# Kernel optimization log

Hardware: AMD Instinct MI355X
Metric: run time of the kernel (lower is better)

## Reference

```python
import jax, jax.numpy as jnp
import numpy as np

NUM_HEADS = 16
ROPE_THETA = 10000.0


def _rotate_half(x):
    d = x.shape[-1] // 2
    return jnp.concatenate((-x[..., d:], x[..., :d]), axis=-1)


def setup_inputs() -> dict:
    key = jax.random.key(0)
    k1, k2, k3, k4 = jax.random.split(key, 4)
    T, HID = 3072, 1024
    hidden_states = jax.random.normal(k1, (T, HID), dtype=jnp.float32)
    w_qkv = jax.random.normal(k2, (HID, 3 * HID), dtype=jnp.float32) * (1.0 / np.sqrt(HID))
    w_o = jax.random.normal(k3, (HID, HID), dtype=jnp.float32) * (1.0 / np.sqrt(HID))
    attention_mask = jnp.zeros((T, T), dtype=jnp.float32)  # additive bias over token pairs
    position_ids = jax.random.randint(k4, (T,), 0, T, dtype=jnp.int32)
    return {
        "hidden_states": hidden_states,
        "w_qkv": w_qkv,
        "w_o": w_o,
        "attention_mask": attention_mask,
        "position_ids": position_ids,
    }


def reference(hidden_states, w_qkv, w_o, attention_mask, position_ids):
    T, hid = hidden_states.shape
    H = NUM_HEADS
    D = hid // H

    # fused QKV projection (bias=False)
    qkv = hidden_states @ w_qkv  # [T, 3*hid]
    q, k, v = jnp.split(qkv, 3, axis=-1)
    q = q.reshape(T, H, D)
    k = k.reshape(T, H, D)
    v = v.reshape(T, H, D)

    # RoPE per packed-token position_ids
    inv_freq = 1.0 / (ROPE_THETA ** (jnp.arange(0, D, 2, dtype=jnp.float32) / D))  # [D/2]
    freqs = position_ids.astype(jnp.float32)[:, None] * inv_freq[None, :]  # [T, D/2]
    emb = jnp.concatenate((freqs, freqs), axis=-1)  # [T, D]
    cos = jnp.cos(emb)[:, None, :]  # [T, 1, D]
    sin = jnp.sin(emb)[:, None, :]
    q = q * cos + _rotate_half(q) * sin
    k = k * cos + _rotate_half(k) * sin

    # dense token-token attention over packed tokens
    scale = 1.0 / np.sqrt(D).astype(np.float32)
    scores = jnp.einsum("thd,shd->hts", q, k) * scale  # [H, T, T]
    scores = scores + attention_mask[None, :, :]
    probs = jax.nn.softmax(scores, axis=-1)
    out = jnp.einsum("hts,shd->thd", probs, v).reshape(T, hid)
    return out @ w_o
```

## Files before the change

kernel.cpp:

```cpp
#include <hip/hip_runtime.h>
#include <hip/hip_bf16.h>
#include <hip/hip_fp16.h>
#include <math.h>

#define T_TOK 3072
#define HID   1024
#define NH    16
#define HD    64
#define KVSPLIT 4
#define KVCHUNK (T_TOK / KVSPLIT)
#define NQB (T_TOK / 128)
#define LOG2E 1.4426950408889634f

typedef __attribute__((ext_vector_type(8))) short bf16x8;
typedef __attribute__((ext_vector_type(8))) unsigned short u16x8;
typedef __attribute__((ext_vector_type(4))) float f32x4;
typedef __attribute__((ext_vector_type(16))) float f32x16;
typedef __attribute__((ext_vector_type(4))) unsigned int u32x4;

#define VMCNT(n) asm volatile("s_waitcnt vmcnt(" #n ")" ::: "memory")
#define SB() __builtin_amdgcn_sched_barrier(0)

static __device__ __forceinline__ unsigned short f2bf(float x) {
  __hip_bfloat16 h = __float2bfloat16(x);
  return __builtin_bit_cast(unsigned short, h);
}
static __device__ __forceinline__ float bf2f(unsigned short u) {
  unsigned int v = (unsigned int)u << 16;
  return __builtin_bit_cast(float, v);
}
static __device__ __forceinline__ unsigned short f2h(float x) {
  __half h = __float2half(x);
  return __builtin_bit_cast(unsigned short, h);
}
static __device__ __forceinline__ float h2f(unsigned short u) {
  __half h = __builtin_bit_cast(__half, u);
  return __half2float(h);
}

static __device__ __forceinline__ int swz(int row, int cb) {
  return row * 64 + ((cb ^ ((row & 7) << 4)) >> 1);
}

__global__ __launch_bounds__(256) void prep(const float* __restrict__ X,
                                            const float* __restrict__ Wqkv,
                                            const float* __restrict__ Wo,
                                            const int* __restrict__ pos,
                                            const float* __restrict__ mask,
                                            unsigned short* __restrict__ Xb,
                                            unsigned short* __restrict__ WqkvT,
                                            unsigned short* __restrict__ WoT,
                                            float* __restrict__ ctab,
                                            float* __restrict__ stab,
                                            int* __restrict__ flags) {
  __shared__ float tile[32][33];
  __shared__ int sflag;
  const int b = blockIdx.x;
  const int tid = threadIdx.x;
  if (b < 3072) {
    int i = (b * 256 + tid) * 4;
    float4 v = *(const float4*)(X + i);
    ushort4 o;
    o.x = f2bf(v.x); o.y = f2bf(v.y); o.z = f2bf(v.z); o.w = f2bf(v.w);
    *(ushort4*)(Xb + i) = o;
  } else if (b < 6144) {
    int b2 = b - 3072;
    int c0 = (b2 % 96) * 32, r0 = (b2 / 96) * 32;
    int tx = tid & 31, ty = tid >> 5;
    #pragma unroll
    for (int i2 = 0; i2 < 32; i2 += 8)
      tile[ty + i2][tx] = Wqkv[(size_t)(r0 + ty + i2) * 3072 + c0 + tx];
    __syncthreads();
    #pragma unroll
    for (int i2 = 0; i2 < 32; i2 += 8)
      WqkvT[(size_t)(c0 + ty + i2) * 1024 + r0 + tx] = f2bf(tile[tx][ty + i2]);
  } else if (b < 7168) {
    int b2 = b - 6144;
    int c0 = (b2 % 32) * 32, r0 = (b2 / 32) * 32;
    int tx = tid & 31, ty = tid >> 5;
    #pragma unroll
    for (int i2 = 0; i2 < 32; i2 += 8)
      tile[ty + i2][tx] = Wo[(size_t)(r0 + ty + i2) * 1024 + c0 + tx];
    __syncthreads();
    #pragma unroll
    for (int i2 = 0; i2 < 32; i2 += 8)
      WoT[(size_t)(c0 + ty + i2) * 1024 + r0 + tx] = f2bf(tile[tx][ty + i2]);
  } else if (b < 7552) {
    int i = (b - 7168) * 256 + tid;
    int t = i >> 5, j = i & 31;
    float inv = expf(-(float)j * 0.28782313662425572f);
    float f = (float)pos[t] * inv;
    ctab[i] = cosf(f);
    stab[i] = sinf(f);
  } else {
    int c = b - 7552;
    int qx = c % NQB, z = c / NQB;
    const float* base = mask + (size_t)(qx * 128) * T_TOK + z * KVCHUNK;
    int any = 0;
    const int NC4 = KVCHUNK / 4;
    for (int i = tid; i < 128 * NC4; i += 256) {
      int row = i / NC4, cc = i - row * NC4;
      float4 v = *(const float4*)(base + (size_t)row * T_TOK + cc * 4);
      any |= (v.x != 0.f) | (v.y != 0.f) | (v.z != 0.f) | (v.w != 0.f);
    }
    if (tid == 0) sflag = 0;
    __syncthreads();
    if (__any(any) && (tid & 63) == 0) sflag = 1;
    __syncthreads();
    if (tid == 0) flags[z * NQB + qx] = sflag;
  }
}

__global__ __launch_bounds__(256) void rope_v(const unsigned short* __restrict__ QKVb,
                                              const float* __restrict__ ctab,
                                              const float* __restrict__ stab,
                                              unsigned short* __restrict__ Qh,
                                              unsigned short* __restrict__ Kh,
                                              unsigned short* __restrict__ Vt) {
  const float QSCL = 0.18033688011112042f;
  const int h = blockIdx.y;
  const int t0 = blockIdx.x * 64;
  const int g = threadIdx.x & 3, tl = threadIdx.x >> 2;
  const int t = t0 + tl;
  __shared__ unsigned short vlds[64][72];

  const size_t rowb = (size_t)t * (3 * HID) + h * HD + g * 8;
  u16x8 qa = *(const u16x8*)(QKVb + rowb);
  u16x8 qb = *(const u16x8*)(QKVb + rowb + 32);
  u16x8 ka = *(const u16x8*)(QKVb + rowb + HID);
  u16x8 kb = *(const u16x8*)(QKVb + rowb + HID + 32);
  u16x8 va = *(const u16x8*)(QKVb + rowb + 2 * HID);
  u16x8 vb = *(const u16x8*)(QKVb + rowb + 2 * HID + 32);

  u16x8 qo0, qo1, ko0, ko1;
  #pragma unroll
  for (int e = 0; e < 8; ++e) {
    int j = g * 8 + e;
    float c = ctab[t * 32 + j], s = stab[t * 32 + j];
    float q1 = bf2f(qa[e]), q2 = bf2f(qb[e]);
    float k1 = bf2f(ka[e]), k2 = bf2f(kb[e]);
    qo0[e] = f2bf((q1 * c - q2 * s) * QSCL);
    qo1[e] = f2bf((q2 * c + q1 * s) * QSCL);
    ko0[e] = f2bf(k1 * c - k2 * s);
    ko1[e] = f2bf(k2 * c + k1 * s);
    vlds[tl][j] = va[e];
    vlds[tl][32 + j] = vb[e];
  }
  size_t ob = ((size_t)h * T_TOK + t) * HD + g * 8;
  *(u16x8*)(Qh + ob) = qo0;
  *(u16x8*)(Qh + ob + 32) = qo1;
  *(u16x8*)(Kh + ob) = ko0;
  *(u16x8*)(Kh + ob + 32) = ko1;

  __syncthreads();
  u16x8 o0, o1;
  #pragma unroll
  for (int e = 0; e < 8; ++e) {
    o0[e] = vlds[g * 16 + e][tl];
    o1[e] = vlds[g * 16 + 8 + e][tl];
  }
  u16x8 w0, w1;
  #pragma unroll
  for (int e = 0; e < 4; ++e) {
    w0[e] = o0[e];     w0[4 + e] = o1[e];
    w1[e] = o0[4 + e]; w1[4 + e] = o1[4 + e];
  }
  size_t vb2 = ((size_t)h * HD + tl) * T_TOK + t0 + g * 16;
  *(u16x8*)(Vt + vb2) = w0;
  *(u16x8*)(Vt + vb2 + 8) = w1;
}

template <int OBF16>
__device__ __forceinline__ void gemm_body(const unsigned short* __restrict__ A,
                                          const unsigned short* __restrict__ Bt,
                                          float* __restrict__ C,
                                          unsigned short* __restrict__ Cb,
                                          int M, int N, int K) {
  __shared__ unsigned short As[2][128 * 32];
  __shared__ unsigned short Bs[2][128 * 32];
  const int lane = threadIdx.x & 63;
  const int wv = threadIdx.x >> 6;
  const int wm = wv >> 1, wn = wv & 1;
  const int r = lane & 15, hi = lane >> 4;
  const int nwg = gridDim.x;
  const int flat = blockIdx.x;
  const int sid = (flat & 7) * (nwg >> 3) + (flat >> 3);
  const int mblocks = M >> 7;
  const int m0 = (sid % mblocks) * 128, n0 = (sid / mblocks) * 128;

  const int srow = lane >> 2;
  const int scb  = ((lane & 3) * 16) ^ ((srow & 3) << 4);
  const unsigned short* ga = A  + (size_t)(m0 + wv * 16 + srow) * K + (scb >> 1);
  const unsigned short* gb = Bt + (size_t)(n0 + wv * 16 + srow) * K + (scb >> 1);
  char* asd = (char*)&As[0][0] + wv * 1024;
  char* bsd = (char*)&Bs[0][0] + wv * 1024;

  auto stage = [&](int buf, int kt) {
    __builtin_amdgcn_global_load_lds(
        (const __attribute__((address_space(1))) unsigned int*)(ga + kt),
        (__attribute__((address_space(3))) unsigned int*)(asd + buf * 8192), 16, 0, 0);
    __builtin_amdgcn_global_load_lds(
        (const __attribute__((address_space(1))) unsigned int*)(ga + (size_t)64 * K + kt),
        (__attribute__((address_space(3))) unsigned int*)(asd + buf * 8192 + 4096), 16, 0, 0);
    __builtin_amdgcn_global_load_lds(
        (const __attribute__((address_space(1))) unsigned int*)(gb + kt),
        (__attribute__((address_space(3))) unsigned int*)(bsd + buf * 8192), 16, 0, 0);
    __builtin_amdgcn_global_load_lds(
        (const __attribute__((address_space(1))) unsigned int*)(gb + (size_t)64 * K + kt),
        (__attribute__((address_space(3))) unsigned int*)(bsd + buf * 8192 + 4096), 16, 0, 0);
  };

  f32x4 acc[4][4] = {};
  const int NT = K >> 5;
  stage(0, 0);
  #pragma unroll 2
  for (int it = 0; it < NT; ++it) {
    const int buf = it & 1;
    if (it + 1 < NT) {
      stage(buf ^ 1, (it + 1) * 32);
      VMCNT(4);
    } else {
      VMCNT(0);
    }
    SB();
    __builtin_amdgcn_s_barrier();
    SB();
    bf16x8 a[4], b[4];
    const int cbs = (hi * 16) ^ ((r & 3) << 4);
    #pragma unroll
    for (int tm = 0; tm < 4; ++tm)
      a[tm] = *(const bf16x8*)&As[buf][(wm * 64 + tm * 16 + r) * 32 + (cbs >> 1)];
    #pragma unroll
    for (int tn = 0; tn < 4; ++tn)
      b[tn] = *(const bf16x8*)&Bs[buf][(wn * 64 + tn * 16 + r) * 32 + (cbs >> 1)];
    #pragma unroll
    for (int tm = 0; tm < 4; ++tm)
      #pragma unroll
      for (int tn = 0; tn < 4; ++tn)
        acc[tm][tn] = __builtin_amdgcn_mfma_f32_16x16x32_bf16(a[tm], b[tn], acc[tm][tn], 0, 0, 0);
    __builtin_amdgcn_s_barrier();
  }
  #pragma unroll
  for (int tm = 0; tm < 4; ++tm)
    #pragma unroll
    for (int tn = 0; tn < 4; ++tn) {
      int colg = n0 + wn * 64 + tn * 16 + r;
      int rowg = m0 + wm * 64 + tm * 16 + hi * 4;
      if (OBF16) {
        unsigned short* cp = Cb + (size_t)rowg * N + colg;
        #pragma unroll
        for (int j = 0; j < 4; ++j) cp[(size_t)j * N] = f2bf(acc[tm][tn][j]);
      } else {
        float* cp = C + (size_t)rowg * N + colg;
        #pragma unroll
        for (int j = 0; j < 4; ++j) cp[(size_t)j * N] = acc[tm][tn][j];
      }
    }
}

__global__ __launch_bounds__(256) void gemm_bt(const unsigned short* __restrict__ A,
                                               const unsigned short* __restrict__ Bt,
                                               float* __restrict__ C, int M, int N, int K) {
  gemm_body<0>(A, Bt, C, nullptr, M, N, K);
}
__global__ __launch_bounds__(256) void gemm_bt_bf16(const unsigned short* __restrict__ A,
                                                    const unsigned short* __restrict__ Bt,
                                                    unsigned short* __restrict__ Cb,
                                                    int M, int N, int K) {
  gemm_body<1>(A, Bt, nullptr, Cb, M, N, K);
}

__global__ __launch_bounds__(256) void flash_attn(const unsigned short* __restrict__ Qh,
                                                  const unsigned short* __restrict__ Kh,
                                                  const unsigned short* __restrict__ Vt,
                                                  const float* __restrict__ mask,
                                                  const int* __restrict__ flags,
                                                  unsigned short* __restrict__ Op,
                                                  float* __restrict__ Mp,
                                                  float* __restrict__ Lp) {
  const int NBLK = NH * NQB * KVSPLIT;
  int id = blockIdx.x;
  int sid = (id & 7) * (NBLK / 8) + (id >> 3);
  const int hh = sid / (NQB * KVSPLIT);
  int rem = sid % (NQB * KVSPLIT);
  const int z  = rem / NQB;
  const int qx = rem % NQB;
  const int q0 = qx * 128;
  const int kv0 = z * KVCHUNK;
  const int NT = KVCHUNK / 64;

  __shared__ unsigned short Ks[2][64 * 64];
  __shared__ unsigned short Vs[2][64 * 64];
  const int lane = threadIdx.x & 63, wv = threadIdx.x >> 6;
  const int q31 = lane & 31, h2 = lane >> 5;
  const int qw = q0 + wv * 32 + q31;

  bf16x8 qf[4];
  #pragma unroll
  for (int ks = 0; ks < 4; ++ks)
    qf[ks] = *(const bf16x8*)(Qh + ((size_t)hh * T_TOK + qw) * HD + ks * 16 + h2 * 8);

  f32x16 acc_o[2] = {};
  const int hasmask = flags[z * NQB + qx];
  float m = hasmask ? -INFINITY : 0.f;
  float l = 0.f;

  const int ldrow = lane >> 3;
  const int colS  = ((lane & 7) * 16) ^ (ldrow << 4);
  const unsigned short* kga = Kh + ((size_t)hh * T_TOK + wv * 16 + ldrow) * HD + (colS >> 1);
  const unsigned short* vga = Vt + ((size_t)hh * HD + wv * 16 + ldrow) * T_TOK + (colS >> 1);
  char* ksd = (char*)&Ks[0][0] + wv * 2048;
  char* vsd = (char*)&Vs[0][0] + wv * 2048;
  const float* mrow = mask + (size_t)qw * T_TOK;

  auto stage = [&](int buf, int s0) {
    __builtin_amdgcn_global_load_lds(
        (const __attribute__((address_space(1))) unsigned int*)(kga + (size_t)s0 * HD),
        (__attribute__((address_space(3))) unsigned int*)(ksd + buf * 8192), 16, 0, 0);
    __builtin_amdgcn_global_load_lds(
        (const __attribute__((address_space(1))) unsigned int*)(kga + (size_t)s0 * HD + 8 * HD),
        (__attribute__((address_space(3))) unsigned int*)(ksd + buf * 8192 + 1024), 16, 0, 0);
    __builtin_amdgcn_global_load_lds(
        (const __attribute__((address_space(1))) unsigned int*)(vga + s0),
        (__attribute__((address_space(3))) unsigned int*)(vsd + buf * 8192), 16, 0, 0);
    __builtin_amdgcn_global_load_lds(
        (const __attribute__((address_space(1))) unsigned int*)(vga + s0 + 8 * T_TOK),
        (__attribute__((address_space(3))) unsigned int*)(vsd + buf * 8192 + 1024), 16, 0, 0);
  };

  float4 mk[8];

  auto qkt = [&](int cur, f32x16& as0, f32x16& as1) {
    __builtin_amdgcn_s_setprio(1);
    #pragma unroll
    for (int ks = 0; ks < 4; ++ks) {
      bf16x8 kf0 = *(const bf16x8*)&Ks[cur][swz(q31,      ks * 32 + h2 * 16)];
      bf16x8 kf1 = *(const bf16x8*)&Ks[cur][swz(32 + q31, ks * 32 + h2 * 16)];
      as0 = __builtin_amdgcn_mfma_f32_32x32x16_bf16(kf0, qf[ks], as0, 0, 0, 0);
      as1 = __builtin_amdgcn_mfma_f32_32x32x16_bf16(kf1, qf[ks], as1, 0, 0, 0);
    }
    __builtin_amdgcn_s_setprio(0);
  };

  auto pv = [&](int cur, const unsigned int* pk) {
    __builtin_amdgcn_s_setprio(1);
    #pragma unroll
    for (int kvb = 0; kvb < 2; ++kvb)
      #pragma unroll
      for (int s = 0; s < 2; ++s) {
        u32x4 fr;
        fr[0] = pk[kvb * 8 + 4 * s + 0];
        fr[1] = pk[kvb * 8 + 4 * s + 1];
        fr[2] = pk[kvb * 8 + 4 * s + 2];
        fr[3] = pk[kvb * 8 + 4 * s + 3];
        bf16x8 pfrag = __builtin_bit_cast(bf16x8, fr);
        #pragma unroll
        for (int db = 0; db < 2; ++db) {
          bf16x8 vf = *(const bf16x8*)&Vs[cur][swz(db * 32 + q31, kvb * 64 + s * 32 + h2 * 16)];
          acc_o[db] = __builtin_amdgcn_mfma_f32_32x32x16_bf16(vf, pfrag, acc_o[db], 0, 0, 0);
        }
      }
    __builtin_amdgcn_s_setprio(0);
  };

  auto tile_nomask = [&](int cur) {
    f32x16 as0 = {}, as1 = {};
    qkt(cur, as0, as1);
    float ps = 0.f;
    unsigned int pk[16];
    #pragma unroll
    for (int kvb = 0; kvb < 2; ++kvb) {
      const f32x16& as = kvb ? as1 : as0;
      #pragma unroll
      for (int j = 0; j < 4; ++j) {
        float e0 = __builtin_amdgcn_exp2f(as[j * 4 + 0]);
        float e1 = __builtin_amdgcn_exp2f(as[j * 4 + 1]);
        float e2 = __builtin_amdgcn_exp2f(as[j * 4 + 2]);
        float e3 = __builtin_amdgcn_exp2f(as[j * 4 + 3]);
        ps += (e0 + e1) + (e2 + e3);
        pk[kvb * 8 + j * 2 + 0] = (unsigned int)f2bf(e0) | ((unsigned int)f2bf(e1) << 16);
        pk[kvb * 8 + j * 2 + 1] = (unsigned int)f2bf(e2) | ((unsigned int)f2bf(e3) << 16);
      }
    }
    l += ps;
    pv(cur, pk);
  };

  auto tile_mask = [&](int cur) {
    f32x16 as0 = {}, as1 = {};
    qkt(cur, as0, as1);
    float sv[2][16];
    #pragma unroll
    for (int reg = 0; reg < 16; ++reg) {
      float m0v = (&mk[0 + (reg >> 2)].x)[reg & 3];
      float m1v = (&mk[4 + (reg >> 2)].x)[reg & 3];
      sv[0][reg] = fmaf(m0v, LOG2E, as0[reg]);
      sv[1][reg] = fmaf(m1v, LOG2E, as1[reg]);
    }
    float p0 = sv[0][0];
    #pragma unroll
    for (int i = 1; i < 16; ++i) p0 = fmaxf(p0, sv[0][i]);
    #pragma unroll
    for (int i = 0; i < 16; ++i) p0 = fmaxf(p0, sv[1][i]);
    float pmax = fmaxf(p0, __shfl_xor(p0, 32));
    if (__any(pmax > m + 8.f)) {
      float mnew = fmaxf(m, pmax);
      float sc = __builtin_amdgcn_exp2f(m - mnew);
      m = mnew;
      l *= sc;
      #pragma unroll
      for (int db = 0; db < 2; ++db)
        #pragma unroll
        for (int i = 0; i < 16; ++i) acc_o[db][i] *= sc;
    }
    float ps = 0.f;
    unsigned int pk[16];
    #pragma unroll
    for (int kvb = 0; kvb < 2; ++kvb)
      #pragma unroll
      for (int j = 0; j < 4; ++j) {
        float e0 = __builtin_amdgcn_exp2f(sv[kvb][j * 4 + 0] - m);
        float e1 = __builtin_amdgcn_exp2f(sv[kvb][j * 4 + 1] - m);
        float e2 = __builtin_amdgcn_exp2f(sv[kvb][j * 4 + 2] - m);
        float e3 = __builtin_amdgcn_exp2f(sv[kvb][j * 4 + 3] - m);
        ps += (e0 + e1) + (e2 + e3);
        pk[kvb * 8 + j * 2 + 0] = (unsigned int)f2bf(e0) | ((unsigned int)f2bf(e1) << 16);
        pk[kvb * 8 + j * 2 + 1] = (unsigned int)f2bf(e2) | ((unsigned int)f2bf(e3) << 16);
      }
    l += ps;
    pv(cur, pk);
  };

  stage(0, kv0);

  if (hasmask) {
    for (int it = 0; it < NT - 1; ++it) {
      const int s0 = kv0 + it * 64;
      #pragma unroll
      for (int kvb = 0; kvb < 2; ++kvb)
        #pragma unroll
        for (int g = 0; g < 4; ++g)
          mk[kvb * 4 + g] = *(const float4*)(mrow + s0 + kvb * 32 + g * 8 + 4 * h2);
      stage((it + 1) & 1, s0 + 64);
      VMCNT(12);
      SB();
      __builtin_amdgcn_s_barrier();
      SB();
      tile_mask(it & 1);
      __builtin_amdgcn_s_barrier();
    }
    const int s0 = kv0 + (NT - 1) * 64;
    #pragma unroll
    for (int kvb = 0; kvb < 2; ++kvb)
      #pragma unroll
      for (int g = 0; g < 4; ++g)
        mk[kvb * 4 + g] = *(const float4*)(mrow + s0 + kvb * 32 + g * 8 + 4 * h2);
    VMCNT(8);
    SB();
    __builtin_amdgcn_s_barrier();
    SB();
    tile_mask((NT - 1) & 1);
  } else {
    for (int it = 0; it < NT - 1; ++it) {
      stage((it + 1) & 1, kv0 + (it + 1) * 64);
      VMCNT(4);
      SB();
      __builtin_amdgcn_s_barrier();
      SB();
      tile_nomask(it & 1);
      __builtin_amdgcn_s_barrier();
    }
    VMCNT(0);
    SB();
    __builtin_amdgcn_s_barrier();
    SB();
    tile_nomask((NT - 1) & 1);
  }

  float lf = l + __shfl_xor(l, 32);
  float lfinv = 1.f / lf;
  unsigned short* oprow = Op + (((size_t)z * T_TOK + qw) * NH + hh) * HD;
  #pragma unroll
  for (int db = 0; db < 2; ++db)
    #pragma unroll
    for (int g = 0; g < 4; ++g) {
      ushort4 o4;
      o4.x = f2h(acc_o[db][g * 4 + 0] * lfinv);
      o4.y = f2h(acc_o[db][g * 4 + 1] * lfinv);
      o4.z = f2h(acc_o[db][g * 4 + 2] * lfinv);
      o4.w = f2h(acc_o[db][g * 4 + 3] * lfinv);
      *(ushort4*)(oprow + db * 32 + g * 8 + 4 * h2) = o4;
    }
  if (h2 == 0) {
    size_t mi = ((size_t)z * T_TOK + qw) * NH + hh;
    Mp[mi] = m;
    Lp[mi] = lf;
  }
}

__global__ __launch_bounds__(256) void combine(const unsigned short* __restrict__ Op,
                                               const float* __restrict__ Mp,
                                               const float* __restrict__ Lp,
                                               unsigned short* __restrict__ Ob) {
  int idx = blockIdx.x * 256 + threadIdx.x;
  int t = idx >> 8;
  int q4 = (idx & 255) * 4;
  int h = q4 >> 6, d = q4 & 63;
  float mz[KVSPLIT], lz[KVSPLIT];
  float ms = -INFINITY;
  #pragma unroll
  for (int zz = 0; zz < KVSPLIT; ++zz) {
    size_t mi = ((size_t)zz * T_TOK + t) * NH + h;
    mz[zz] = Mp[mi];
    lz[zz] = Lp[mi];
    ms = fmaxf(ms, mz[zz]);
  }
  float lsum = 0.f;
  float wl[KVSPLIT];
  #pragma unroll
  for (int zz = 0; zz < KVSPLIT; ++zz) {
    wl[zz] = lz[zz] * __builtin_amdgcn_exp2f(mz[zz] - ms);
    lsum += wl[zz];
  }
  float4 o = {0.f, 0.f, 0.f, 0.f};
  #pragma unroll
  for (int zz = 0; zz < KVSPLIT; ++zz) {
    ushort4 p = *(const ushort4*)(Op + (((size_t)zz * T_TOK + t) * NH + h) * HD + d);
    o.x += h2f(p.x) * wl[zz]; o.y += h2f(p.y) * wl[zz];
    o.z += h2f(p.z) * wl[zz]; o.w += h2f(p.w) * wl[zz];
  }
  float inv = 1.f / lsum;
  ushort4 ob;
  ob.x = f2bf(o.x * inv); ob.y = f2bf(o.y * inv);
  ob.z = f2bf(o.z * inv); ob.w = f2bf(o.w * inv);
  *(ushort4*)(Ob + (size_t)t * HID + q4) = ob;
}

extern "C" void kernel_launch(void* const* d_in, const int* in_sizes, int n_in,
                              void* d_out, int out_size, void* d_ws, size_t ws_size,
                              hipStream_t stream) {
  const float* X    = (const float*)d_in[0];
  const float* Wqkv = (const float*)d_in[1];
  const float* Wo   = (const float*)d_in[2];
  const float* mask = (const float*)d_in[3];
  const int*   pos  = (const int*)d_in[4];
  float* out = (float*)d_out;

  char* ws = (char*)d_ws;
  size_t off = 0;
  auto alloc = [&](size_t bytes) {
    char* p = ws + off;
    off += (bytes + 255) & ~(size_t)255;
    return p;
  };
  unsigned short* Xb    = (unsigned short*)alloc((size_t)T_TOK * HID * 2);
  unsigned short* WqkvT = (unsigned short*)alloc((size_t)3 * HID * HID * 2);
  unsigned short* WoT   = (unsigned short*)alloc((size_t)HID * HID * 2);
  unsigned short* Qh    = (unsigned short*)alloc((size_t)NH * T_TOK * HD * 2);
  unsigned short* Kh    = (unsigned short*)alloc((size_t)NH * T_TOK * HD * 2);
  unsigned short* Vt    = (unsigned short*)alloc((size_t)NH * HD * T_TOK * 2);
  unsigned short* Ob    = (unsigned short*)alloc((size_t)T_TOK * HID * 2);
  float*          ctab  = (float*)alloc((size_t)T_TOK * 32 * 4);
  float*          stab  = (float*)alloc((size_t)T_TOK * 32 * 4);
  float*          Mp    = (float*)alloc((size_t)KVSPLIT * T_TOK * NH * 4);
  float*          Lp    = (float*)alloc((size_t)KVSPLIT * T_TOK * NH * 4);
  int*            flags = (int*)alloc((size_t)KVSPLIT * NQB * 4);
  char*           region = alloc((size_t)KVSPLIT * T_TOK * HID * 2);
  unsigned short* QKVb  = (unsigned short*)region;
  unsigned short* Op    = (unsigned short*)region;

  prep<<<7648, 256, 0, stream>>>(X, Wqkv, Wo, pos, mask, Xb, WqkvT, WoT, ctab, stab, flags);

  gemm_bt_bf16<<<dim3((3 * HID / 128) * (T_TOK / 128)), 256, 0, stream>>>(Xb, WqkvT, QKVb, T_TOK, 3 * HID, HID);

  rope_v<<<dim3(T_TOK / 64, NH), 256, 0, stream>>>(QKVb, ctab, stab, Qh, Kh, Vt);

  flash_attn<<<dim3(NH * NQB * KVSPLIT), 256, 0, stream>>>(Qh, Kh, Vt, mask, flags, Op, Mp, Lp);
  combine<<<T_TOK, 256, 0, stream>>>(Op, Mp, Lp, Ob);

  gemm_bt<<<dim3((HID / 128) * (T_TOK / 128)), 256, 0, stream>>>(Ob, WoT, out, T_TOK, HID, HID);
}
```

Measured before the change: 159.8 us.

## Split flash attention into separate no-mask and mask kernels with tighter occupancy

Splits the single flash attention kernel into a no-mask kernel and a mask kernel, each launched over the full grid, with blocks exiting early when the per-tile flag does not match. The no-mask kernel asks for 6 blocks per CU via launch bounds, single-buffers V, and splits the wait so V loads overlap the QK^T and softmax phase. The aim is to cut register and LDS pressure on the common zero-mask path and raise occupancy. In exchange it adds an extra kernel launch whose blocks mostly exit immediately, plus an additional barrier per tile.

```diff
diff --git a/kernel.cpp b/kernel.cpp
--- a/kernel.cpp
+++ b/kernel.cpp
@@ -270,7 +270,157 @@
   gemm_body<1>(A, Bt, nullptr, Cb, M, N, K);
 }
 
-__global__ __launch_bounds__(256) void flash_attn(const unsigned short* __restrict__ Qh,
+__global__ __launch_bounds__(256, 6) void flash_nomask(const unsigned short* __restrict__ Qh,
+                                                       const unsigned short* __restrict__ Kh,
+                                                       const unsigned short* __restrict__ Vt,
+                                                       const int* __restrict__ flags,
+                                                       unsigned short* __restrict__ Op,
+                                                       float* __restrict__ Mp,
+                                                       float* __restrict__ Lp) {
+  const int NBLK = NH * NQB * KVSPLIT;
+  int id = blockIdx.x;
+  int sid = (id & 7) * (NBLK / 8) + (id >> 3);
+  const int hh = sid / (NQB * KVSPLIT);
+  int rem = sid % (NQB * KVSPLIT);
+  const int z  = rem / NQB;
+  const int qx = rem % NQB;
+  if (flags[z * NQB + qx]) return;
+  const int q0 = qx * 128;
+  const int kv0 = z * KVCHUNK;
+  const int NT = KVCHUNK / 64;
+
+  __shared__ unsigned short Ks[2][64 * 64];
+  __shared__ unsigned short Vs[64 * 64];
+  const int lane = threadIdx.x & 63, wv = threadIdx.x >> 6;
+  const int q31 = lane & 31, h2 = lane >> 5;
+  const int qw = q0 + wv * 32 + q31;
+
+  bf16x8 qf[4];
+  #pragma unroll
+  for (int ks = 0; ks < 4; ++ks)
+    qf[ks] = *(const bf16x8*)(Qh + ((size_t)hh * T_TOK + qw) * HD + ks * 16 + h2 * 8);
+
+  f32x16 acc_o[2] = {};
+  float l = 0.f;
+
+  const int ldrow = lane >> 3;
+  const int colS  = ((lane & 7) * 16) ^ (ldrow << 4);
+  const unsigned short* kga = Kh + ((size_t)hh * T_TOK + wv * 16 + ldrow) * HD + (colS >> 1);
+  const unsigned short* vga = Vt + ((size_t)hh * HD + wv * 16 + ldrow) * T_TOK + (colS >> 1);
+  char* ksd = (char*)&Ks[0][0] + wv * 2048;
+  char* vsd = (char*)&Vs[0] + wv * 2048;
+
+  auto stageK = [&](int buf, int s0) {
+    __builtin_amdgcn_global_load_lds(
+        (const __attribute__((address_space(1))) unsigned int*)(kga + (size_t)s0 * HD),
+        (__attribute__((address_space(3))) unsigned int*)(ksd + buf * 8192), 16, 0, 0);
+    __builtin_amdgcn_global_load_lds(
+        (const __attribute__((address_space(1))) unsigned int*)(kga + (size_t)s0 * HD + 8 * HD),
+        (__attribute__((address_space(3))) unsigned int*)(ksd + buf * 8192 + 1024), 16, 0, 0);
+  };
+  auto stageV = [&](int s0) {
+    __builtin_amdgcn_global_load_lds(
+        (const __attribute__((address_space(1))) unsigned int*)(vga + s0),
+        (__attribute__((address_space(3))) unsigned int*)vsd, 16, 0, 0);
+    __builtin_amdgcn_global_load_lds(
+        (const __attribute__((address_space(1))) unsigned int*)(vga + s0 + 8 * T_TOK),
+        (__attribute__((address_space(3))) unsigned int*)(vsd + 1024), 16, 0, 0);
+  };
+
+  stageK(0, kv0);
+
+  for (int it = 0; it < NT; ++it) {
+    const int s0 = kv0 + it * 64;
+    const int cur = it & 1;
+    stageV(s0);
+    if (it + 1 < NT) {
+      stageK(cur ^ 1, s0 + 64);
+      VMCNT(4);
+    } else {
+      VMCNT(2);
+    }
+    SB();
+    __builtin_amdgcn_s_barrier();
+    SB();
+
+    f32x16 as0 = {}, as1 = {};
+    __builtin_amdgcn_s_setprio(1);
+    #pragma unroll
+    for (int ks = 0; ks < 4; ++ks) {
+      bf16x8 kf0 = *(const bf16x8*)&Ks[cur][swz(q31,      ks * 32 + h2 * 16)];
+      bf16x8 kf1 = *(const bf16x8*)&Ks[cur][swz(32 + q31, ks * 32 + h2 * 16)];
+      as0 = __builtin_amdgcn_mfma_f32_32x32x16_bf16(kf0, qf[ks], as0, 0, 0, 0);
+      as1 = __builtin_amdgcn_mfma_f32_32x32x16_bf16(kf1, qf[ks], as1, 0, 0, 0);
+    }
+    __builtin_amdgcn_s_setprio(0);
+
+    float ps = 0.f;
+    unsigned int pk[16];
+    #pragma unroll
+    for (int kvb = 0; kvb < 2; ++kvb) {
+      const f32x16& as = kvb ? as1 : as0;
+      #pragma unroll
+      for (int j = 0; j < 4; ++j) {
+        float e0 = __builtin_amdgcn_exp2f(as[j * 4 + 0]);
+        float e1 = __builtin_amdgcn_exp2f(as[j * 4 + 1]);
+        float e2 = __builtin_amdgcn_exp2f(as[j * 4 + 2]);
+        float e3 = __builtin_amdgcn_exp2f(as[j * 4 + 3]);
+        ps += (e0 + e1) + (e2 + e3);
+        pk[kvb * 8 + j * 2 + 0] = (unsigned int)f2bf(e0) | ((unsigned int)f2bf(e1) << 16);
+        pk[kvb * 8 + j * 2 + 1] = (unsigned int)f2bf(e2) | ((unsigned int)f2bf(e3) << 16);
+      }
+    }
+    l += ps;
+
+    if (it + 1 < NT) VMCNT(2); else VMCNT(0);
+    SB();
+    __builtin_amdgcn_s_barrier();
+    SB();
+
+    __builtin_amdgcn_s_setprio(1);
+    #pragma unroll
+    for (int kvb = 0; kvb < 2; ++kvb)
+      #pragma unroll
+      for (int s = 0; s < 2; ++s) {
+        u32x4 fr;
+        fr[0] = pk[kvb * 8 + 4 * s + 0];
+        fr[1] = pk[kvb * 8 + 4 * s + 1];
+        fr[2] = pk[kvb * 8 + 4 * s + 2];
+        fr[3] = pk[kvb * 8 + 4 * s + 3];
+        bf16x8 pfrag = __builtin_bit_cast(bf16x8, fr);
+        #pragma unroll
+        for (int db = 0; db < 2; ++db) {
+          bf16x8 vf = *(const bf16x8*)&Vs[swz(db * 32 + q31, kvb * 64 + s * 32 + h2 * 16)];
+          acc_o[db] = __builtin_amdgcn_mfma_f32_32x32x16_bf16(vf, pfrag, acc_o[db], 0, 0, 0);
+        }
+      }
+    __builtin_amdgcn_s_setprio(0);
+
+    __builtin_amdgcn_s_barrier();
+  }
+
+  float lf = l + __shfl_xor(l, 32);
+  float lfinv = 1.f / lf;
+  unsigned short* oprow = Op + (((size_t)z * T_TOK + qw) * NH + hh) * HD;
+  #pragma unroll
+  for (int db = 0; db < 2; ++db)
+    #pragma unroll
+    for (int g = 0; g < 4; ++g) {
+      ushort4 o4;
+      o4.x = f2h(acc_o[db][g * 4 + 0] * lfinv);
+      o4.y = f2h(acc_o[db][g * 4 + 1] * lfinv);
+      o4.z = f2h(acc_o[db][g * 4 + 2] * lfinv);
+      o4.w = f2h(acc_o[db][g * 4 + 3] * lfinv);
+      *(ushort4*)(oprow + db * 32 + g * 8 + 4 * h2) = o4;
+    }
+  if (h2 == 0) {
+    size_t mi = ((size_t)z * T_TOK + qw) * NH + hh;
+    Mp[mi] = 0.f;
+    Lp[mi] = lf;
+  }
+}
+
+__global__ __launch_bounds__(256) void flash_mask(const unsigned short* __restrict__ Qh,
                                                   const unsigned short* __restrict__ Kh,
                                                   const unsigned short* __restrict__ Vt,
                                                   const float* __restrict__ mask,
@@ -285,6 +435,7 @@
   int rem = sid % (NQB * KVSPLIT);
   const int z  = rem / NQB;
   const int qx = rem % NQB;
+  if (!flags[z * NQB + qx]) return;
   const int q0 = qx * 128;
   const int kv0 = z * KVCHUNK;
   const int NT = KVCHUNK / 64;
@@ -301,9 +452,7 @@
     qf[ks] = *(const bf16x8*)(Qh + ((size_t)hh * T_TOK + qw) * HD + ks * 16 + h2 * 8);
 
   f32x16 acc_o[2] = {};
-  const int hasmask = flags[z * NQB + qx];
-  float m = hasmask ? -INFINITY : 0.f;
-  float l = 0.f;
+  float m = -INFINITY, l = 0.f;
 
   const int ldrow = lane >> 3;
   const int colS  = ((lane & 7) * 16) ^ (ldrow << 4);
@@ -330,7 +479,8 @@
 
   float4 mk[8];
 
-  auto qkt = [&](int cur, f32x16& as0, f32x16& as1) {
+  auto tile_mask = [&](int cur) {
+    f32x16 as0 = {}, as1 = {};
     __builtin_amdgcn_s_setprio(1);
     #pragma unroll
     for (int ks = 0; ks < 4; ++ks) {
@@ -340,9 +490,47 @@
       as1 = __builtin_amdgcn_mfma_f32_32x32x16_bf16(kf1, qf[ks], as1, 0, 0, 0);
     }
     __builtin_amdgcn_s_setprio(0);
-  };
-
-  auto pv = [&](int cur, const unsigned int* pk) {
+
+    float sv[2][16];
+    #pragma unroll
+    for (int reg = 0; reg < 16; ++reg) {
+      float m0v = (&mk[0 + (reg >> 2)].x)[reg & 3];
+      float m1v = (&mk[4 + (reg >> 2)].x)[reg & 3];
+      sv[0][reg] = fmaf(m0v, LOG2E, as0[reg]);
+      sv[1][reg] = fmaf(m1v, LOG2E, as1[reg]);
+    }
+    float p0 = sv[0][0];
+    #pragma unroll
+    for (int i = 1; i < 16; ++i) p0 = fmaxf(p0, sv[0][i]);
+    #pragma unroll
+    for (int i = 0; i < 16; ++i) p0 = fmaxf(p0, sv[1][i]);
+    float pmax = fmaxf(p0, __shfl_xor(p0, 32));
+    if (__any(pmax > m + 8.f)) {
+      float mnew = fmaxf(m, pmax);
+      float sc = __builtin_amdgcn_exp2f(m - mnew);
+      m = mnew;
+      l *= sc;
+      #pragma unroll
+      for (int db = 0; db < 2; ++db)
+        #pragma unroll
+        for (int i = 0; i < 16; ++i) acc_o[db][i] *= sc;
+    }
+    float ps = 0.f;
+    unsigned int pk[16];
+    #pragma unroll
+    for (int kvb = 0; kvb < 2; ++kvb)
+      #pragma unroll
+      for (int j = 0; j < 4; ++j) {
+        float e0 = __builtin_amdgcn_exp2f(sv[kvb][j * 4 + 0] - m);
+        float e1 = __builtin_amdgcn_exp2f(sv[kvb][j * 4 + 1] - m);
+        float e2 = __builtin_amdgcn_exp2f(sv[kvb][j * 4 + 2] - m);
+        float e3 = __builtin_amdgcn_exp2f(sv[kvb][j * 4 + 3] - m);
+        ps += (e0 + e1) + (e2 + e3);
+        pk[kvb * 8 + j * 2 + 0] = (unsigned int)f2bf(e0) | ((unsigned int)f2bf(e1) << 16);
+        pk[kvb * 8 + j * 2 + 1] = (unsigned int)f2bf(e2) | ((unsigned int)f2bf(e3) << 16);
+      }
+    l += ps;
+
     __builtin_amdgcn_s_setprio(1);
     #pragma unroll
     for (int kvb = 0; kvb < 2; ++kvb)
@@ -363,119 +551,34 @@
     __builtin_amdgcn_s_setprio(0);
   };
 
-  auto tile_nomask = [&](int cur) {
-    f32x16 as0 = {}, as1 = {};
-    qkt(cur, as0, as1);
-    float ps = 0.f;
-    unsigned int pk[16];
-    #pragma unroll
-    for (int kvb = 0; kvb < 2; ++kvb) {
-      const f32x16& as = kvb ? as1 : as0;
-      #pragma unroll
-      for (int j = 0; j < 4; ++j) {
-        float e0 = __builtin_amdgcn_exp2f(as[j * 4 + 0]);
-        float e1 = __builtin_amdgcn_exp2f(as[j * 4 + 1]);
-        float e2 = __builtin_amdgcn_exp2f(as[j * 4 + 2]);
-        float e3 = __builtin_amdgcn_exp2f(as[j * 4 + 3]);
-        ps += (e0 + e1) + (e2 + e3);
-        pk[kvb * 8 + j * 2 + 0] = (unsigned int)f2bf(e0) | ((unsigned int)f2bf(e1) << 16);
-        pk[kvb * 8 + j * 2 + 1] = (unsigned int)f2bf(e2) | ((unsigned int)f2bf(e3) << 16);
-      }
-    }
-    l += ps;
-    pv(cur, pk);
-  };
-
-  auto tile_mask = [&](int cur) {
-    f32x16 as0 = {}, as1 = {};
-    qkt(cur, as0, as1);
-    float sv[2][16];
-    #pragma unroll
-    for (int reg = 0; reg < 16; ++reg) {
-      float m0v = (&mk[0 + (reg >> 2)].x)[reg & 3];
-      float m1v = (&mk[4 + (reg >> 2)].x)[reg & 3];
-      sv[0][reg] = fmaf(m0v, LOG2E, as0[reg]);
-      sv[1][reg] = fmaf(m1v, LOG2E, as1[reg]);
-    }
-    float p0 = sv[0][0];
-    #pragma unroll
-    for (int i = 1; i < 16; ++i) p0 = fmaxf(p0, sv[0][i]);
-    #pragma unroll
-    for (int i = 0; i < 16; ++i) p0 = fmaxf(p0, sv[1][i]);
-    float pmax = fmaxf(p0, __shfl_xor(p0, 32));
-    if (__any(pmax > m + 8.f)) {
-      float mnew = fmaxf(m, pmax);
-      float sc = __builtin_amdgcn_exp2f(m - mnew);
-      m = mnew;
-      l *= sc;
-      #pragma unroll
-      for (int db = 0; db < 2; ++db)
-        #pragma unroll
-        for (int i = 0; i < 16; ++i) acc_o[db][i] *= sc;
-    }
-    float ps = 0.f;
-    unsigned int pk[16];
-    #pragma unroll
-    for (int kvb = 0; kvb < 2; ++kvb)
-      #pragma unroll
-      for (int j = 0; j < 4; ++j) {
-        float e0 = __builtin_amdgcn_exp2f(sv[kvb][j * 4 + 0] - m);
-        float e1 = __builtin_amdgcn_exp2f(sv[kvb][j * 4 + 1] - m);
-        float e2 = __builtin_amdgcn_exp2f(sv[kvb][j * 4 + 2] - m);
-        float e3 = __builtin_amdgcn_exp2f(sv[kvb][j * 4 + 3] - m);
-        ps += (e0 + e1) + (e2 + e3);
-        pk[kvb * 8 + j * 2 + 0] = (unsigned int)f2bf(e0) | ((unsigned int)f2bf(e1) << 16);
-        pk[kvb * 8 + j * 2 + 1] = (unsigned int)f2bf(e2) | ((unsigned int)f2bf(e3) << 16);
-      }
-    l += ps;
-    pv(cur, pk);
-  };
-
   stage(0, kv0);
 
-  if (hasmask) {
-    for (int it = 0; it < NT - 1; ++it) {
-      const int s0 = kv0 + it * 64;
-      #pragma unroll
-      for (int kvb = 0; kvb < 2; ++kvb)
-        #pragma unroll
-        for (int g = 0; g < 4; ++g)
-          mk[kvb * 4 + g] = *(const float4*)(mrow + s0 + kvb * 32 + g * 8 + 4 * h2);
-      stage((it + 1) & 1, s0 + 64);
-      VMCNT(12);
-      SB();
-      __builtin_amdgcn_s_barrier();
-      SB();
-      tile_mask(it & 1);
-      __builtin_amdgcn_s_barrier();
-    }
-    const int s0 = kv0 + (NT - 1) * 64;
+  for (int it = 0; it < NT - 1; ++it) {
+    const int s0 = kv0 + it * 64;
     #pragma unroll
     for (int kvb = 0; kvb < 2; ++kvb)
       #pragma unroll
       for (int g = 0; g < 4; ++g)
         mk[kvb * 4 + g] = *(const float4*)(mrow + s0 + kvb * 32 + g * 8 + 4 * h2);
-    VMCNT(8);
+    stage((it + 1) & 1, s0 + 64);
+    VMCNT(12);
     SB();
     __builtin_amdgcn_s_barrier();
     SB();
-    tile_mask((NT - 1) & 1);
-  } else {
-    for (int it = 0; it < NT - 1; ++it) {
-      stage((it + 1) & 1, kv0 + (it + 1) * 64);
-      VMCNT(4);
-      SB();
-      __builtin_amdgcn_s_barrier();
-      SB();
-      tile_nomask(it & 1);
-      __builtin_amdgcn_s_barrier();
-    }
-    VMCNT(0);
-    SB();
+    tile_mask(it & 1);
     __builtin_amdgcn_s_barrier();
-    SB();
-    tile_nomask((NT - 1) & 1);
-  }
+  }
+  const int s0l = kv0 + (NT - 1) * 64;
+  #pragma unroll
+  for (int kvb = 0; kvb < 2; ++kvb)
+    #pragma unroll
+    for (int g = 0; g < 4; ++g)
+      mk[kvb * 4 + g] = *(const float4*)(mrow + s0l + kvb * 32 + g * 8 + 4 * h2);
+  VMCNT(8);
+  SB();
+  __builtin_amdgcn_s_barrier();
+  SB();
+  tile_mask((NT - 1) & 1);
 
   float lf = l + __shfl_xor(l, 32);
   float lfinv = 1.f / lf;
@@ -575,7 +678,8 @@
 
   rope_v<<<dim3(T_TOK / 64, NH), 256, 0, stream>>>(QKVb, ctab, stab, Qh, Kh, Vt);
 
-  flash_attn<<<dim3(NH * NQB * KVSPLIT), 256, 0, stream>>>(Qh, Kh, Vt, mask, flags, Op, Mp, Lp);
+  flash_nomask<<<dim3(NH * NQB * KVSPLIT), 256, 0, stream>>>(Qh, Kh, Vt, flags, Op, Mp, Lp);
+  flash_mask<<<dim3(NH * NQB * KVSPLIT), 256, 0, stream>>>(Qh, Kh, Vt, mask, flags, Op, Mp, Lp);
   combine<<<T_TOK, 256, 0, stream>>>(Op, Mp, Lp, Ob);
 
   gemm_bt<<<dim3((HID / 128) * (T_TOK / 128)), 256, 0, stream>>>(Ob, WoT, out, T_TOK, HID, HID);
```

New measurement: 194.7 us. 21.8% more time.
